# Kernel tuning notes

Measured on AMD Instinct MI355X. Metric: run time of the kernel, lower is better.

## Reference

```python
import jax, jax.numpy as jnp
import numpy as np

TAU = 2.0          # LIF tau
V_TH = 1.0         # threshold, v_reset = 0
EPS = 1e-5         # BN eps
NUM_HEADS = 12
PATCH = 4
LENTH = 64         # (H/p)*(W/p)


def _heaviside(x):
    return (x >= 0.0).astype(x.dtype)


def lif(x_seq):
    """Multi-step LIF (decay_input=True, hard reset to 0). x_seq: [T, ...] -> spikes [T, ...]."""
    def step(v, x):
        v = v + (x - v) / TAU
        s = _heaviside(v - V_TH)
        v = v * (1.0 - s)
        return v, s
    _, s_seq = jax.lax.scan(step, jnp.zeros_like(x_seq[0]), x_seq)
    return s_seq


def bn_eval(x, gamma, beta, mean, var):
    # x: [T,B,C,H,W]; eval-mode BN over channel axis 2
    sh = (1, 1, -1, 1, 1)
    inv = gamma.reshape(sh) / jnp.sqrt(var.reshape(sh) + EPS)
    return (x - mean.reshape(sh)) * inv + beta.reshape(sh)


def setup_inputs() -> dict:
    key = jax.random.key(0)
    ks = jax.random.split(key, 8)
    T, B, C, H, W = 4, 8, 384, 32, 32
    p = PATCH
    x = jax.random.normal(ks[0], (T, B, C, H, W), jnp.float32)
    w_conv = jax.random.normal(ks[1], (2 * C, C, p, p), jnp.float32) / np.sqrt(C * p * p)
    w_proj = jax.random.normal(ks[2], (C, C), jnp.float32) / np.sqrt(C)
    bn1_gamma = 0.5 + jax.random.uniform(ks[3], (2 * C,), jnp.float32)
    bn1_beta = 0.1 * jax.random.normal(ks[4], (2 * C,), jnp.float32)
    bn1_mean = 0.1 * jax.random.normal(ks[5], (2 * C,), jnp.float32)
    bn1_var = 0.5 + jax.random.uniform(ks[6], (2 * C,), jnp.float32)
    bn2_gamma = 0.5 + jax.random.uniform(jax.random.fold_in(key, 10), (C,), jnp.float32)
    bn2_beta = 0.1 * jax.random.normal(jax.random.fold_in(key, 11), (C,), jnp.float32)
    bn2_mean = 0.1 * jax.random.normal(jax.random.fold_in(key, 12), (C,), jnp.float32)
    bn2_var = 0.5 + jax.random.uniform(jax.random.fold_in(key, 13), (C,), jnp.float32)
    fr_x = 0.05 + 0.5 * jax.random.uniform(jax.random.fold_in(key, 14), (1, 1, NUM_HEADS, 1, 1), jnp.float32)
    fr_attn = 0.05 + 0.5 * jax.random.uniform(jax.random.fold_in(key, 15), (1, 1, NUM_HEADS, 1, 1), jnp.float32)
    return dict(x=x, w_conv=w_conv, bn1_gamma=bn1_gamma, bn1_beta=bn1_beta,
                bn1_mean=bn1_mean, bn1_var=bn1_var, w_proj=w_proj,
                bn2_gamma=bn2_gamma, bn2_beta=bn2_beta, bn2_mean=bn2_mean,
                bn2_var=bn2_var, fr_x=fr_x, fr_attn=fr_attn)


def reference(x, w_conv, bn1_gamma, bn1_beta, bn1_mean, bn1_var, w_proj,
              bn2_gamma, bn2_beta, bn2_mean, bn2_var, fr_x, fr_attn):
    T, B, C, H, W = x.shape
    h = NUM_HEADS
    Ch = C // h
    p = PATCH
    x_feat = x
    xs = lif(x)                                           # [T,B,C,H,W] spikes
    # patchify conv (kernel=stride=p, no bias), flatten T*B for the conv
    y = jax.lax.conv_general_dilated(
        xs.reshape(T * B, C, H, W), w_conv, (p, p), 'VALID',
        dimension_numbers=('NCHW', 'OIHW', 'NCHW'))
    Hp, Wp = H // p, W // p
    y = bn_eval(y.reshape(T, B, 2 * C, Hp, Wp), bn1_gamma, bn1_beta, bn1_mean, bn1_var)
    y = y.reshape(T, B, h, 2 * Ch, Hp * Wp)
    y1, y2 = y[:, :, :, :Ch, :], y[:, :, :, Ch:, :]       # [T,B,h,Ch,N']
    xr = xs.reshape(T, B, h, Ch, H * W)                   # [T,B,h,Ch,N]
    scale1 = 1.0 / jnp.sqrt(fr_x * Ch)                    # [1,1,h,1,1]
    attn = jnp.einsum('tbhdp,tbhdn->tbhpn', y1, xr) * scale1   # [T,B,h,N',N]
    attn = lif(attn)
    scale2 = 1.0 / jnp.sqrt(fr_attn * LENTH)
    out = jnp.einsum('tbhdp,tbhpn->tbhdn', y2, attn) * scale2  # [T,B,h,Ch,N]
    out = lif(out.reshape(T, B, C, H, W))
    out = jnp.einsum('tbchw,oc->tbohw', out, w_proj)      # 1x1 conv, no bias
    out = bn_eval(out, bn2_gamma, bn2_beta, bn2_mean, bn2_var)
    return out + x_feat
```

## Files before the change

kernel.cpp:

```cpp
#include <hip/hip_runtime.h>
#include <math.h>

#define TT 4
#define BB 8
#define CC 384
#define HWN 1024
#define NHEAD 12
#define CHD 32
#define C2 768
#define LL 64
#define KCONV 6144
#define KB_TOT 192
#define MROWS 2048

#define K2INV ((_Float16)4.8828125e-4f)

typedef _Float16 f16x8 __attribute__((ext_vector_type(8)));
typedef _Float16 f16x4 __attribute__((ext_vector_type(4)));
typedef float f32x4 __attribute__((ext_vector_type(4)));

#if defined(__has_builtin)
#if __has_builtin(__builtin_amdgcn_global_load_lds)
#define USE_GLL 1
#endif
#endif
#ifndef USE_GLL
#define USE_GLL 0
#endif

#if USE_GLL
typedef __attribute__((address_space(3))) unsigned int lds_uint;
typedef const __attribute__((address_space(1))) unsigned int glob_uint;
__device__ __forceinline__ void load_lds16(const void* g, void* l) {
    __builtin_amdgcn_global_load_lds((glob_uint*)g, (lds_uint*)l, 16, 0, 0);
}
#endif

__global__ __launch_bounds__(256) void k_pack(const float* __restrict__ w,
                                              _Float16* __restrict__ W0,
                                              _Float16* __restrict__ W1) {
    int g = blockIdx.x * 256 + threadIdx.x;
    int o = g * 8;
    int kbnb = o >> 12;
    int kb = kbnb / 6;
    int nb = kbnb - kb * 6;
    int q = (o >> 10) & 3;
    int col = (o >> 3) & 127;
    int k = kb * 32 + q * 8;
    int n = nb * 128 + col;
    const float* src = w + (size_t)n * KCONV + k;
    f16x8 h, l;
#pragma unroll
    for (int j = 0; j < 8; j++) {
        float wv = src[j];
        _Float16 hi = (_Float16)wv;
        float rem = (wv - (float)hi) * 2048.0f;
        h[j] = hi;
        l[j] = (_Float16)rem;
    }
    *(f16x8*)(W0 + o) = h;
    *(f16x8*)(W1 + o) = l;
}

__global__ __launch_bounds__(256) void k_pack_wp(const float* __restrict__ wp,
                                                 _Float16* __restrict__ WpH) {
    int g = blockIdx.x * 256 + threadIdx.x;
    int o8 = g * 8;
    int kbot = o8 >> 12;
    int kb = kbot / 3;
    int ot = kbot - kb * 3;
    int q = (o8 >> 10) & 3;
    int row = (o8 >> 3) & 127;
    int o = ot * 128 + row;
    int c = kb * 32 + q * 8;
    const float* src = wp + (size_t)o * CC + c;
    f16x8 h;
#pragma unroll
    for (int j = 0; j < 8; j++) h[j] = (_Float16)src[j];
    *(f16x8*)(WpH + o8) = h;
}

__global__ __launch_bounds__(256) void k_lif1(const float* __restrict__ x,
                                              _Float16* __restrict__ xsC,
                                              _Float16* __restrict__ xsF) {
    int nt = blockIdx.x & 3, q8 = blockIdx.x >> 2;
    int bh = blockIdx.y;
    int b = bh / NHEAD, hh = bh % NHEAD;
    int n = nt * 256 + threadIdx.x;
    const int stride = BB * CC * HWN;
    int h = n >> 5, w = n & 31;
    int pi = h >> 2, a = h & 3, pj = w >> 2, bp = w & 3;
    int rowp = pi * 8 + pj;
    int qa = a >> 1;
    int jc = (a & 1) * 4 + bp;
    size_t base0 = ((size_t)b * CC + hh * 32 + q8 * 8) * HWN + n;
    f16x8 frag[4];
#pragma unroll
    for (int j = 0; j < 8; j++) {
        int c = hh * 32 + q8 * 8 + j;
        int kb = c >> 1;
        int qc = (c & 1) * 2 + qa;
        size_t cbase = (size_t)kb * 4096 + qc * 1024 + jc;
        float v = 0.0f;
        size_t off = base0 + (size_t)j * HWN;
#pragma unroll
        for (int t = 0; t < TT; t++) {
            float xv = x[(size_t)t * stride + off];
            v += (xv - v) * 0.5f;
            float s = (v >= 1.0f) ? 1.0f : 0.0f;
            if (s > 0.0f) v = 0.0f;
            frag[t][j] = (_Float16)s;
            int tb = t * BB + b;
            int mt = tb >> 1;
            int row = (tb & 1) * 64 + rowp;
            xsC[(size_t)mt * (192 * 4096) + cbase + (size_t)row * 8] = (_Float16)s;
        }
    }
#pragma unroll
    for (int t = 0; t < TT; t++) {
        int tb = t * BB + b;
        size_t dst = ((size_t)(tb * NHEAD + hh) * 8 + (n >> 7)) * 4096 + q8 * 1024 + (size_t)(n & 127) * 8;
        *(f16x8*)(xsF + dst) = frag[t];
    }
}

__global__ __launch_bounds__(256, 2) void k_conv_mfma(const _Float16* __restrict__ xsC,
                                                      const _Float16* __restrict__ W0,
                                                      const _Float16* __restrict__ W1,
                                                      float* __restrict__ P,
                                                      int kbPerSplit) {
    __shared__ __align__(16) _Float16 As[2][4096];
    __shared__ __align__(16) _Float16 Bh[2][4096];
    __shared__ __align__(16) _Float16 Bl[2][4096];

    int mt = blockIdx.x;
    int nt = blockIdx.y;
    int s = blockIdx.z;
    int kb0 = s * kbPerSplit;
    int tid = threadIdx.x;
    int wave = tid >> 6;
    int lane = tid & 63;
    int l16 = lane & 15, lq = lane >> 4;
    int wr = (wave & 1) * 64, wc = (wave >> 1) * 64;

    f32x4 acc[4][4];
#pragma unroll
    for (int i = 0; i < 4; i++)
#pragma unroll
        for (int j = 0; j < 4; j++) acc[i][j] = (f32x4){0.f, 0.f, 0.f, 0.f};

    const char* aBase = (const char*)xsC + (size_t)mt * (192 * 8192);
    const char* b0Base = (const char*)W0 + (size_t)nt * 8192;
    const char* b1Base = (const char*)W1 + (size_t)nt * 8192;
    int wo = wave * 2048;
    int lo16 = lane * 16;

#if USE_GLL
#define STAGE(buf, kb) do {                                              \
    const char* aS = aBase + (size_t)(kb) * 8192;                        \
    const char* b0S = b0Base + (size_t)(kb) * (6 * 8192);                \
    const char* b1S = b1Base + (size_t)(kb) * (6 * 8192);                \
    load_lds16(aS + wo + lo16, (char*)As[buf] + wo);                     \
    load_lds16(aS + wo + 1024 + lo16, (char*)As[buf] + wo + 1024);       \
    load_lds16(b0S + wo + lo16, (char*)Bh[buf] + wo);                    \
    load_lds16(b0S + wo + 1024 + lo16, (char*)Bh[buf] + wo + 1024);      \
    load_lds16(b1S + wo + lo16, (char*)Bl[buf] + wo);                    \
    load_lds16(b1S + wo + 1024 + lo16, (char*)Bl[buf] + wo + 1024);      \
} while (0)
#else
#define STAGE(buf, kb) do {                                              \
    const char* aS = aBase + (size_t)(kb) * 8192;                        \
    const char* b0S = b0Base + (size_t)(kb) * (6 * 8192);                \
    const char* b1S = b1Base + (size_t)(kb) * (6 * 8192);                \
    _Pragma("unroll")                                                    \
    for (int i_ = 0; i_ < 2; ++i_) {                                     \
        int off_ = wo + i_ * 1024 + lo16;                                \
        *(float4*)((char*)As[buf] + off_) = *(const float4*)(aS + off_); \
        *(float4*)((char*)Bh[buf] + off_) = *(const float4*)(b0S + off_);\
        *(float4*)((char*)Bl[buf] + off_) = *(const float4*)(b1S + off_);\
    }                                                                    \
} while (0)
#endif

    STAGE(0, kb0);
    __syncthreads();

    int cur = 0;
    for (int i = 0; i < kbPerSplit; ++i) {
        if (i + 1 < kbPerSplit) STAGE(cur ^ 1, kb0 + i + 1);

        f16x8 af[4], afs[4], bf[4];
#pragma unroll
        for (int fi = 0; fi < 4; fi++) {
            af[fi] = *(const f16x8*)&As[cur][(size_t)(lq * 128 + wr + fi * 16 + l16) * 8];
            afs[fi] = af[fi] * K2INV;
        }
#pragma unroll
        for (int fj = 0; fj < 4; fj++)
            bf[fj] = *(const f16x8*)&Bh[cur][(size_t)(lq * 128 + wc + fj * 16 + l16) * 8];
#pragma unroll
        for (int fi = 0; fi < 4; fi++)
#pragma unroll
            for (int fj = 0; fj < 4; fj++)
                acc[fi][fj] = __builtin_amdgcn_mfma_f32_16x16x32_f16(af[fi], bf[fj], acc[fi][fj], 0, 0, 0);
#pragma unroll
        for (int fj = 0; fj < 4; fj++)
            bf[fj] = *(const f16x8*)&Bl[cur][(size_t)(lq * 128 + wc + fj * 16 + l16) * 8];
#pragma unroll
        for (int fi = 0; fi < 4; fi++)
#pragma unroll
            for (int fj = 0; fj < 4; fj++)
                acc[fi][fj] = __builtin_amdgcn_mfma_f32_16x16x32_f16(afs[fi], bf[fj], acc[fi][fj], 0, 0, 0);

        __syncthreads();
        cur ^= 1;
    }
#undef STAGE

    size_t Pbase = (size_t)s * MROWS * C2;
#pragma unroll
    for (int fi = 0; fi < 4; fi++)
#pragma unroll
        for (int fj = 0; fj < 4; fj++) {
            int ccol = nt * 128 + wc + fj * 16 + l16;
#pragma unroll
            for (int r = 0; r < 4; r++) {
                int rr = mt * 128 + wr + fi * 16 + lq * 4 + r;
                P[Pbase + (size_t)rr * C2 + ccol] = acc[fi][fj][r];
            }
        }
}

__global__ __launch_bounds__(256) void k_reduce_frag(const float* __restrict__ P,
                                                     const float* __restrict__ g1,
                                                     const float* __restrict__ b1,
                                                     const float* __restrict__ m1,
                                                     const float* __restrict__ v1,
                                                     _Float16* __restrict__ A1,
                                                     _Float16* __restrict__ A2,
                                                     int KS) {
    __shared__ float y2ls[32][66];
    int tb = blockIdx.x / NHEAD, hh = blockIdx.x % NHEAD;
    int tid = threadIdx.x;
    int pp = tid >> 2, cq = (tid & 3) * 16;

    size_t rowbase = ((size_t)tb * 64 + pp) * C2 + hh * 64 + cq;
    float yv[16];
#pragma unroll
    for (int i = 0; i < 16; i++) yv[i] = 0.0f;
    for (int s = 0; s < KS; s++) {
        const float* p = P + (size_t)s * MROWS * C2 + rowbase;
#pragma unroll
        for (int i4 = 0; i4 < 4; i4++) {
            float4 v = *(const float4*)(p + i4 * 4);
            yv[i4 * 4 + 0] += v.x;
            yv[i4 * 4 + 1] += v.y;
            yv[i4 * 4 + 2] += v.z;
            yv[i4 * 4 + 3] += v.w;
        }
    }
#pragma unroll
    for (int i = 0; i < 16; i++) {
        int oc = hh * 64 + cq + i;
        float inv = g1[oc] / sqrtf(v1[oc] + 1e-5f);
        yv[i] = (yv[i] - m1[oc]) * inv + b1[oc];
    }

    size_t reg = (size_t)(tb * NHEAD + hh) * 4096;
    if (cq < 32) {
#pragma unroll
        for (int gi = 0; gi < 2; gi++) {
            int c0 = cq + gi * 8;
            f16x8 h, l;
#pragma unroll
            for (int j = 0; j < 8; j++) {
                float v = yv[gi * 8 + j];
                _Float16 hi = (_Float16)v;
                h[j] = hi;
                l[j] = (_Float16)((v - (float)hi) * 2048.0f);
            }
            size_t a = reg + (size_t)(((pp >> 4) * 4 + (c0 >> 3)) * 128 + (pp & 15) * 8);
            *(f16x8*)(A1 + a) = h;
            *(f16x8*)(A1 + a + 2048) = l;
        }
    } else {
#pragma unroll
        for (int i = 0; i < 16; i++) y2ls[cq - 32 + i][pp] = yv[i];
    }
    __syncthreads();
    int d16 = tid & 15, grp = tid >> 4;
    f16x8 h, l;
#pragma unroll
    for (int j = 0; j < 8; j++) {
        float v = y2ls[(grp >> 3) * 16 + d16][((grp >> 2) & 1) * 32 + (grp & 3) * 8 + j];
        _Float16 hi = (_Float16)v;
        h[j] = hi;
        l[j] = (_Float16)((v - (float)hi) * 2048.0f);
    }
    size_t a = reg + (size_t)((grp * 16 + d16) * 8);
    *(f16x8*)(A2 + a) = h;
    *(f16x8*)(A2 + a + 2048) = l;
}

__global__ __launch_bounds__(256) void k_attn_mfma(const _Float16* __restrict__ xsF,
                                                   const _Float16* __restrict__ A1,
                                                   const _Float16* __restrict__ A2,
                                                   const float* __restrict__ fr_x,
                                                   const float* __restrict__ fr_attn,
                                                   _Float16* __restrict__ OsF) {
    __shared__ __align__(16) _Float16 Bs[4][128][8];
    __shared__ __align__(16) _Float16 Sat[8][128][8];

    int nt = blockIdx.x;
    int bh = blockIdx.y;
    int b = bh / NHEAD, hh = bh % NHEAD;
    int tid = threadIdx.x;
    int w = tid >> 6;
    int lane = tid & 63;
    int l16 = lane & 15, lq = lane >> 4;

    float scale1 = 1.0f / sqrtf(fr_x[hh] * 32.0f);
    float scale2 = 1.0f / sqrtf(fr_attn[hh] * 64.0f);

    float va[8][4];
    float vo[2][2][4];
#pragma unroll
    for (int nf = 0; nf < 8; nf++)
#pragma unroll
        for (int r = 0; r < 4; r++) va[nf][r] = 0.0f;
#pragma unroll
    for (int dt = 0; dt < 2; dt++)
#pragma unroll
        for (int nf = 0; nf < 2; nf++)
#pragma unroll
            for (int r = 0; r < 4; r++) vo[dt][nf][r] = 0.0f;

    for (int t = 0; t < TT; t++) {
        int tb = t * BB + b;
        size_t reg = (size_t)(tb * NHEAD + hh);
        const char* src = (const char*)(xsF + (reg * 8 + nt) * 4096);
#if USE_GLL
        load_lds16(src + tid * 16, (char*)&Bs[0][0][0] + tid * 16);
        load_lds16(src + tid * 16 + 4096, (char*)&Bs[0][0][0] + tid * 16 + 4096);
#else
        *(float4*)((char*)&Bs[0][0][0] + tid * 16) = *(const float4*)(src + tid * 16);
        *(float4*)((char*)&Bs[0][0][0] + tid * 16 + 4096) = *(const float4*)(src + tid * 16 + 4096);
#endif
        const _Float16* a1b = A1 + reg * 4096;
        f16x8 a1h = *(const f16x8*)(a1b + (size_t)(((w * 4 + lq) * 16 + l16) * 8));
        f16x8 a1l = *(const f16x8*)(a1b + 2048 + (size_t)(((w * 4 + lq) * 16 + l16) * 8));
        f16x8 a1ls = a1l * K2INV;
        __syncthreads();

        f32x4 ah[8];
#pragma unroll
        for (int nf = 0; nf < 8; nf++) ah[nf] = (f32x4){0.f, 0.f, 0.f, 0.f};
#pragma unroll
        for (int nf = 0; nf < 8; nf++) {
            f16x8 bf = *(const f16x8*)&Bs[lq][nf * 16 + l16][0];
            ah[nf] = __builtin_amdgcn_mfma_f32_16x16x32_f16(a1h, bf, ah[nf], 0, 0, 0);
            ah[nf] = __builtin_amdgcn_mfma_f32_16x16x32_f16(a1ls, bf, ah[nf], 0, 0, 0);
        }
        int pq = w * 2 + (lq >> 1);
#pragma unroll
        for (int nf = 0; nf < 8; nf++) {
            f16x4 sp;
#pragma unroll
            for (int r = 0; r < 4; r++) {
                float a = ah[nf][r] * scale1;
                float v = va[nf][r];
                v += (a - v) * 0.5f;
                float s = (v >= 1.0f) ? 1.0f : 0.0f;
                va[nf][r] = (s > 0.0f) ? 0.0f : v;
                sp[r] = (_Float16)s;
            }
            *(f16x4*)&Sat[pq][nf * 16 + l16][(lq & 1) * 4] = sp;
        }
        __syncthreads();

        const _Float16* a2b = A2 + reg * 4096;
        f32x4 oh[2][2];
#pragma unroll
        for (int dt = 0; dt < 2; dt++)
#pragma unroll
            for (int nf = 0; nf < 2; nf++) oh[dt][nf] = (f32x4){0.f, 0.f, 0.f, 0.f};
#pragma unroll
        for (int ks = 0; ks < 2; ks++) {
            f16x8 bf0 = *(const f16x8*)&Sat[ks * 4 + lq][w * 32 + l16][0];
            f16x8 bf1 = *(const f16x8*)&Sat[ks * 4 + lq][w * 32 + 16 + l16][0];
#pragma unroll
            for (int dt = 0; dt < 2; dt++) {
                size_t ao = (size_t)(((dt * 8 + ks * 4 + lq) * 16 + l16) * 8);
                f16x8 a2h = *(const f16x8*)(a2b + ao);
                f16x8 a2ls = *(const f16x8*)(a2b + 2048 + ao) * K2INV;
                oh[dt][0] = __builtin_amdgcn_mfma_f32_16x16x32_f16(a2h, bf0, oh[dt][0], 0, 0, 0);
                oh[dt][0] = __builtin_amdgcn_mfma_f32_16x16x32_f16(a2ls, bf0, oh[dt][0], 0, 0, 0);
                oh[dt][1] = __builtin_amdgcn_mfma_f32_16x16x32_f16(a2h, bf1, oh[dt][1], 0, 0, 0);
                oh[dt][1] = __builtin_amdgcn_mfma_f32_16x16x32_f16(a2ls, bf1, oh[dt][1], 0, 0, 0);
            }
        }
        _Float16* og = OsF + (reg * 8 + nt) * 4096;
#pragma unroll
        for (int dt = 0; dt < 2; dt++)
#pragma unroll
            for (int nf = 0; nf < 2; nf++) {
                f16x4 sp;
#pragma unroll
                for (int r = 0; r < 4; r++) {
                    float a = oh[dt][nf][r] * scale2;
                    float v = vo[dt][nf][r];
                    v += (a - v) * 0.5f;
                    float s = (v >= 1.0f) ? 1.0f : 0.0f;
                    vo[dt][nf][r] = (s > 0.0f) ? 0.0f : v;
                    sp[r] = (_Float16)s;
                }
                int n = w * 32 + nf * 16 + l16;
                *(f16x4*)(og + (size_t)((dt * 2 + (lq >> 1)) * 1024 + n * 8 + (lq & 1) * 4)) = sp;
            }
        __syncthreads();
    }
}

__global__ __launch_bounds__(256) void k_proj_mfma(const _Float16* __restrict__ OsF,
                                                   const _Float16* __restrict__ WpH,
                                                   const float* __restrict__ g2,
                                                   const float* __restrict__ b2,
                                                   const float* __restrict__ m2,
                                                   const float* __restrict__ vv2,
                                                   const float* __restrict__ x,
                                                   float* __restrict__ out) {
    __shared__ __align__(16) _Float16 Bs[4][128][8];

    int nt = blockIdx.x;
    int ot = blockIdx.y;
    int tb = blockIdx.z;
    int tid = threadIdx.x;
    int wave = tid >> 6;
    int lane = tid & 63;
    int l16 = lane & 15, lq = lane >> 4;
    int wr = (wave & 1) * 64, wc = (wave >> 1) * 64;

    f32x4 acc[4][4];
#pragma unroll
    for (int i = 0; i < 4; i++)
#pragma unroll
        for (int j = 0; j < 4; j++) acc[i][j] = (f32x4){0.f, 0.f, 0.f, 0.f};

    for (int kb = 0; kb < 12; ++kb) {
        __syncthreads();
        const char* src = (const char*)(OsF + ((size_t)(tb * NHEAD + kb) * 8 + nt) * 4096);
#if USE_GLL
#pragma unroll
        for (int i = 0; i < 2; ++i) {
            int off = (tid + i * 256) * 16;
            load_lds16(src + off, (char*)&Bs[0][0][0] + off);
        }
#else
#pragma unroll
        for (int i = 0; i < 2; ++i) {
            int off = (tid + i * 256) * 16;
            *(float4*)((char*)&Bs[0][0][0] + off) = *(const float4*)(src + off);
        }
#endif
        const _Float16* wbase = WpH + (size_t)(kb * 3 + ot) * 4096 + lq * 1024;
        f16x8 af[4];
#pragma unroll
        for (int fi = 0; fi < 4; fi++)
            af[fi] = *(const f16x8*)(wbase + (size_t)(wr + fi * 16 + l16) * 8);
        __syncthreads();

        f16x8 bf[4];
#pragma unroll
        for (int fj = 0; fj < 4; fj++)
            bf[fj] = *(const f16x8*)&Bs[lq][wc + fj * 16 + l16][0];
#pragma unroll
        for (int fi = 0; fi < 4; fi++)
#pragma unroll
            for (int fj = 0; fj < 4; fj++)
                acc[fi][fj] = __builtin_amdgcn_mfma_f32_16x16x32_f16(af[fi], bf[fj], acc[fi][fj], 0, 0, 0);
    }

    size_t orow_base = (size_t)tb * CC * HWN;
    int n_base = nt * 128 + wc;
#pragma unroll
    for (int fi = 0; fi < 4; fi++) {
        float invv[4], muv[4], btv[4];
#pragma unroll
        for (int r = 0; r < 4; r++) {
            int o = ot * 128 + wr + fi * 16 + lq * 4 + r;
            invv[r] = g2[o] / sqrtf(vv2[o] + 1e-5f);
            muv[r] = m2[o];
            btv[r] = b2[o];
        }
#pragma unroll
        for (int fj = 0; fj < 4; fj++) {
#pragma unroll
            for (int r = 0; r < 4; r++) {
                int o = ot * 128 + wr + fi * 16 + lq * 4 + r;
                size_t addr = orow_base + (size_t)o * HWN + n_base + fj * 16 + l16;
                out[addr] = (acc[fi][fj][r] - muv[r]) * invv[r] + btv[r] + x[addr];
            }
        }
    }
}

extern "C" void kernel_launch(void* const* d_in, const int* in_sizes, int n_in,
                              void* d_out, int out_size, void* d_ws, size_t ws_size,
                              hipStream_t stream) {
    const float* x = (const float*)d_in[0];
    const float* w_conv = (const float*)d_in[1];
    const float* bn1_gamma = (const float*)d_in[2];
    const float* bn1_beta = (const float*)d_in[3];
    const float* bn1_mean = (const float*)d_in[4];
    const float* bn1_var = (const float*)d_in[5];
    const float* w_proj = (const float*)d_in[6];
    const float* bn2_gamma = (const float*)d_in[7];
    const float* bn2_beta = (const float*)d_in[8];
    const float* bn2_mean = (const float*)d_in[9];
    const float* bn2_var = (const float*)d_in[10];
    const float* fr_x = (const float*)d_in[11];
    const float* fr_attn = (const float*)d_in[12];

    const size_t FRAG = (size_t)16 * 192 * 4096 * 2;
    const size_t AB = (size_t)TT * BB * NHEAD * 4096 * 2;
    const size_t WB = (size_t)KCONV * C2 * 2;
    const size_t WPB = (size_t)CC * CC * 2;
    const size_t PB = (size_t)MROWS * C2 * 4;
    _Float16* xsC = (_Float16*)d_ws;
    _Float16* xsF = (_Float16*)((char*)xsC + FRAG);
    _Float16* OsF = (_Float16*)((char*)xsF + FRAG);
    _Float16* A1 = (_Float16*)((char*)OsF + FRAG);
    _Float16* A2 = (_Float16*)((char*)A1 + AB);
    _Float16* W0 = (_Float16*)((char*)A2 + AB);
    _Float16* W1 = (_Float16*)((char*)W0 + WB);
    _Float16* WpH = (_Float16*)((char*)W1 + WB);
    char* tail = (char*)WpH + WPB;

    int KS;
    float* P;
    if (ws_size >= (size_t)(tail - (char*)d_ws) + 8 * PB) {
        KS = 8;
        P = (float*)tail;
    } else if (ws_size >= (size_t)(tail - (char*)d_ws) + 4 * PB) {
        KS = 4;
        P = (float*)tail;
    } else {
        KS = 2;
        P = (float*)OsF;
    }
    int kbPerSplit = KB_TOT / KS;

    k_pack<<<(KCONV * C2 / 8) / 256, 256, 0, stream>>>(w_conv, W0, W1);
    k_pack_wp<<<(CC * CC / 8) / 256, 256, 0, stream>>>(w_proj, WpH);
    k_lif1<<<dim3(16, BB * NHEAD), 256, 0, stream>>>(x, xsC, xsF);
    k_conv_mfma<<<dim3(16, 6, KS), 256, 0, stream>>>(xsC, W0, W1, P, kbPerSplit);
    k_reduce_frag<<<32 * NHEAD, 256, 0, stream>>>(P, bn1_gamma, bn1_beta, bn1_mean, bn1_var, A1, A2, KS);
    k_attn_mfma<<<dim3(8, BB * NHEAD), 256, 0, stream>>>(xsF, A1, A2, fr_x, fr_attn, OsF);
    k_proj_mfma<<<dim3(8, 3, 32), 256, 0, stream>>>(OsF, WpH, bn2_gamma, bn2_beta, bn2_mean, bn2_var, x, (float*)d_out);
}
```

Before: 133.3 us.

## Swap MFMA operand roles for vectorized stores and double-buffer projection GEMM

The conv GEMM swaps its A/B operands so each lane's accumulator covers four consecutive output channels, which allows float4 stores to the partial buffer in place of scalar strided writes. The projection kernel is changed the same way, so the BN2 and residual epilogue reads x and writes out as float4. The projection kernel also double-buffers its LDS tile, prefetches the next weight fragments into registers, and adds a launch-bounds occupancy hint. The aim is to cut store and load instruction counts and to overlap global loads with MFMA work, at the cost of extra registers for the prefetched fragments.

```diff
diff --git a/kernel.cpp b/kernel.cpp
--- a/kernel.cpp
+++ b/kernel.cpp
@@ -189,28 +189,28 @@
     for (int i = 0; i < kbPerSplit; ++i) {
         if (i + 1 < kbPerSplit) STAGE(cur ^ 1, kb0 + i + 1);
 
-        f16x8 af[4], afs[4], bf[4];
-#pragma unroll
-        for (int fi = 0; fi < 4; fi++) {
-            af[fi] = *(const f16x8*)&As[cur][(size_t)(lq * 128 + wr + fi * 16 + l16) * 8];
-            afs[fi] = af[fi] * K2INV;
-        }
-#pragma unroll
-        for (int fj = 0; fj < 4; fj++)
-            bf[fj] = *(const f16x8*)&Bh[cur][(size_t)(lq * 128 + wc + fj * 16 + l16) * 8];
+        f16x8 wf[4], sf[4], sfs[4];
+#pragma unroll
+        for (int fj = 0; fj < 4; fj++) {
+            sf[fj] = *(const f16x8*)&As[cur][(size_t)(lq * 128 + wr + fj * 16 + l16) * 8];
+            sfs[fj] = sf[fj] * K2INV;
+        }
 #pragma unroll
         for (int fi = 0; fi < 4; fi++)
+            wf[fi] = *(const f16x8*)&Bh[cur][(size_t)(lq * 128 + wc + fi * 16 + l16) * 8];
+#pragma unroll
+        for (int fi = 0; fi < 4; fi++)
 #pragma unroll
             for (int fj = 0; fj < 4; fj++)
-                acc[fi][fj] = __builtin_amdgcn_mfma_f32_16x16x32_f16(af[fi], bf[fj], acc[fi][fj], 0, 0, 0);
-#pragma unroll
-        for (int fj = 0; fj < 4; fj++)
-            bf[fj] = *(const f16x8*)&Bl[cur][(size_t)(lq * 128 + wc + fj * 16 + l16) * 8];
+                acc[fi][fj] = __builtin_amdgcn_mfma_f32_16x16x32_f16(wf[fi], sf[fj], acc[fi][fj], 0, 0, 0);
 #pragma unroll
         for (int fi = 0; fi < 4; fi++)
+            wf[fi] = *(const f16x8*)&Bl[cur][(size_t)(lq * 128 + wc + fi * 16 + l16) * 8];
+#pragma unroll
+        for (int fi = 0; fi < 4; fi++)
 #pragma unroll
             for (int fj = 0; fj < 4; fj++)
-                acc[fi][fj] = __builtin_amdgcn_mfma_f32_16x16x32_f16(afs[fi], bf[fj], acc[fi][fj], 0, 0, 0);
+                acc[fi][fj] = __builtin_amdgcn_mfma_f32_16x16x32_f16(wf[fi], sfs[fj], acc[fi][fj], 0, 0, 0);
 
         __syncthreads();
         cur ^= 1;
@@ -219,16 +219,14 @@
 
     size_t Pbase = (size_t)s * MROWS * C2;
 #pragma unroll
-    for (int fi = 0; fi < 4; fi++)
+    for (int fi = 0; fi < 4; fi++) {
+        int oc0 = nt * 128 + wc + fi * 16 + lq * 4;
 #pragma unroll
         for (int fj = 0; fj < 4; fj++) {
-            int ccol = nt * 128 + wc + fj * 16 + l16;
-#pragma unroll
-            for (int r = 0; r < 4; r++) {
-                int rr = mt * 128 + wr + fi * 16 + lq * 4 + r;
-                P[Pbase + (size_t)rr * C2 + ccol] = acc[fi][fj][r];
-            }
-        }
+            int m = mt * 128 + wr + fj * 16 + l16;
+            *(f32x4*)(P + Pbase + (size_t)m * C2 + oc0) = acc[fi][fj];
+        }
+    }
 }
 
 __global__ __launch_bounds__(256) void k_reduce_frag(const float* __restrict__ P,
@@ -421,15 +419,15 @@
     }
 }
 
-__global__ __launch_bounds__(256) void k_proj_mfma(const _Float16* __restrict__ OsF,
-                                                   const _Float16* __restrict__ WpH,
-                                                   const float* __restrict__ g2,
-                                                   const float* __restrict__ b2,
-                                                   const float* __restrict__ m2,
-                                                   const float* __restrict__ vv2,
-                                                   const float* __restrict__ x,
-                                                   float* __restrict__ out) {
-    __shared__ __align__(16) _Float16 Bs[4][128][8];
+__global__ __launch_bounds__(256, 2) void k_proj_mfma(const _Float16* __restrict__ OsF,
+                                                      const _Float16* __restrict__ WpH,
+                                                      const float* __restrict__ g2,
+                                                      const float* __restrict__ b2,
+                                                      const float* __restrict__ m2,
+                                                      const float* __restrict__ vv2,
+                                                      const float* __restrict__ x,
+                                                      float* __restrict__ out) {
+    __shared__ __align__(16) _Float16 Bs[2][4096];
 
     int nt = blockIdx.x;
     int ot = blockIdx.y;
@@ -438,7 +436,7 @@
     int wave = tid >> 6;
     int lane = tid & 63;
     int l16 = lane & 15, lq = lane >> 4;
-    int wr = (wave & 1) * 64, wc = (wave >> 1) * 64;
+    int wn = (wave & 1) * 64, wo = (wave >> 1) * 64;
 
     f32x4 acc[4][4];
 #pragma unroll
@@ -446,60 +444,78 @@
 #pragma unroll
         for (int j = 0; j < 4; j++) acc[i][j] = (f32x4){0.f, 0.f, 0.f, 0.f};
 
+    const char* bBase = (const char*)(OsF + ((size_t)tb * NHEAD * 8 + nt) * 4096);
+    const _Float16* aBase = WpH + (size_t)ot * 4096 + lq * 1024 + (size_t)(wo + l16) * 8;
+    int halfo = wave * 2048;
+    int lo16 = lane * 16;
+
+#if USE_GLL
+#define PSTAGE(buf, kb) do {                                                   \
+    const char* bS = bBase + (size_t)(kb) * (8 * 8192);                        \
+    load_lds16(bS + halfo + lo16, (char*)Bs[buf] + halfo);                     \
+    load_lds16(bS + halfo + 1024 + lo16, (char*)Bs[buf] + halfo + 1024);       \
+} while (0)
+#else
+#define PSTAGE(buf, kb) do {                                                   \
+    const char* bS = bBase + (size_t)(kb) * (8 * 8192);                        \
+    _Pragma("unroll")                                                          \
+    for (int i_ = 0; i_ < 2; ++i_) {                                           \
+        int off_ = halfo + i_ * 1024 + lo16;                                   \
+        *(float4*)((char*)Bs[buf] + off_) = *(const float4*)(bS + off_);       \
+    }                                                                          \
+} while (0)
+#endif
+
+    f16x8 af[4], afn[4];
+#pragma unroll
+    for (int fo = 0; fo < 4; fo++) af[fo] = *(const f16x8*)(aBase + (size_t)(fo * 16) * 8);
+    PSTAGE(0, 0);
+    __syncthreads();
+
+    int cur = 0;
     for (int kb = 0; kb < 12; ++kb) {
+        int kbn = (kb + 1 < 12) ? kb + 1 : kb;
+        if (kb + 1 < 12) PSTAGE(cur ^ 1, kb + 1);
+        const _Float16* an = aBase + (size_t)kbn * (3 * 4096);
+#pragma unroll
+        for (int fo = 0; fo < 4; fo++) afn[fo] = *(const f16x8*)(an + (size_t)(fo * 16) * 8);
+
+        f16x8 bf[4];
+#pragma unroll
+        for (int fn = 0; fn < 4; fn++)
+            bf[fn] = *(const f16x8*)&Bs[cur][(size_t)(lq * 128 + wn + fn * 16 + l16) * 8];
+#pragma unroll
+        for (int fn = 0; fn < 4; fn++)
+#pragma unroll
+            for (int fo = 0; fo < 4; fo++)
+                acc[fn][fo] = __builtin_amdgcn_mfma_f32_16x16x32_f16(bf[fn], af[fo], acc[fn][fo], 0, 0, 0);
+
         __syncthreads();
-        const char* src = (const char*)(OsF + ((size_t)(tb * NHEAD + kb) * 8 + nt) * 4096);
-#if USE_GLL
-#pragma unroll
-        for (int i = 0; i < 2; ++i) {
-            int off = (tid + i * 256) * 16;
-            load_lds16(src + off, (char*)&Bs[0][0][0] + off);
-        }
-#else
-#pragma unroll
-        for (int i = 0; i < 2; ++i) {
-            int off = (tid + i * 256) * 16;
-            *(float4*)((char*)&Bs[0][0][0] + off) = *(const float4*)(src + off);
-        }
-#endif
-        const _Float16* wbase = WpH + (size_t)(kb * 3 + ot) * 4096 + lq * 1024;
-        f16x8 af[4];
-#pragma unroll
-        for (int fi = 0; fi < 4; fi++)
-            af[fi] = *(const f16x8*)(wbase + (size_t)(wr + fi * 16 + l16) * 8);
-        __syncthreads();
-
-        f16x8 bf[4];
-#pragma unroll
-        for (int fj = 0; fj < 4; fj++)
-            bf[fj] = *(const f16x8*)&Bs[lq][wc + fj * 16 + l16][0];
-#pragma unroll
-        for (int fi = 0; fi < 4; fi++)
-#pragma unroll
-            for (int fj = 0; fj < 4; fj++)
-                acc[fi][fj] = __builtin_amdgcn_mfma_f32_16x16x32_f16(af[fi], bf[fj], acc[fi][fj], 0, 0, 0);
-    }
+        cur ^= 1;
+#pragma unroll
+        for (int fo = 0; fo < 4; fo++) af[fo] = afn[fo];
+    }
+#undef PSTAGE
 
     size_t orow_base = (size_t)tb * CC * HWN;
-    int n_base = nt * 128 + wc;
-#pragma unroll
-    for (int fi = 0; fi < 4; fi++) {
-        float invv[4], muv[4], btv[4];
-#pragma unroll
-        for (int r = 0; r < 4; r++) {
-            int o = ot * 128 + wr + fi * 16 + lq * 4 + r;
-            invv[r] = g2[o] / sqrtf(vv2[o] + 1e-5f);
-            muv[r] = m2[o];
-            btv[r] = b2[o];
-        }
-#pragma unroll
-        for (int fj = 0; fj < 4; fj++) {
-#pragma unroll
-            for (int r = 0; r < 4; r++) {
-                int o = ot * 128 + wr + fi * 16 + lq * 4 + r;
-                size_t addr = orow_base + (size_t)o * HWN + n_base + fj * 16 + l16;
-                out[addr] = (acc[fi][fj][r] - muv[r]) * invv[r] + btv[r] + x[addr];
-            }
+#pragma unroll
+    for (int fo = 0; fo < 4; fo++) {
+        int o = ot * 128 + wo + fo * 16 + l16;
+        float inv = g2[o] / sqrtf(vv2[o] + 1e-5f);
+        float mu = m2[o];
+        float bt = b2[o];
+        size_t obase = orow_base + (size_t)o * HWN;
+#pragma unroll
+        for (int fn = 0; fn < 4; fn++) {
+            size_t addr = obase + (size_t)(nt * 128 + wn + fn * 16 + lq * 4);
+            float4 xv = *(const float4*)(x + addr);
+            f32x4 a = acc[fn][fo];
+            float4 ov;
+            ov.x = (a[0] - mu) * inv + bt + xv.x;
+            ov.y = (a[1] - mu) * inv + bt + xv.y;
+            ov.z = (a[2] - mu) * inv + bt + xv.z;
+            ov.w = (a[3] - mu) * inv + bt + xv.w;
+            *(float4*)(out + addr) = ov;
         }
     }
 }
```

Result: no change. 131.1 us (-1.6%).
